# Optimization experiments

Hardware: AMD Instinct MI355X
Metric: run time of the kernel (lower is better)

Reference implementation:

```python
import jax, jax.numpy as jnp
import numpy as np

N_CODES = 4096
D = 256


def setup_inputs() -> dict:
    key = jax.random.key(0)
    k_v, k_w = jax.random.split(key)
    v = jax.random.normal(k_v, (8, 2048, D), dtype=jnp.float32)
    # Embedding init ~ N(0,1), then softmax over dim=1, then row 0 set to 1/d (empty feature)
    w = jax.random.normal(k_w, (N_CODES, D), dtype=jnp.float32)
    w = jax.nn.softmax(w, axis=1)
    w = w.at[0].set(1.0 / D)
    return {"v": v, "vectors": w}


def reference(v, vectors):
    n, d = vectors.shape
    cb = vectors[1:]  # exclude the fixed empty feature at index 0
    # ||v - c||^2 = ||v||^2 - 2 v.c + ||c||^2  (avoids [..., n, d] intermediate)
    v2 = jnp.sum(v * v, axis=-1, keepdims=True)              # [..., 1]
    c2 = jnp.sum(cb * cb, axis=-1)                           # [n-1]
    diff = v2 - 2.0 * jnp.einsum('...d,nd->...n', v, cb) + c2  # [..., n-1]
    idx = jnp.argmin(diff, axis=-1) + 1                      # [...]
    # empty-feature mask: any component differs from 1/d
    mask = jnp.any(v != (1.0 / d), axis=-1)
    idx = jnp.where(mask, idx, 0)
    out = vectors[idx]                                       # gather == onehot @ vectors
    loss = jnp.mean(jnp.square(out - jax.lax.stop_gradient(v)))
    used = jnp.array(0, dtype=jnp.int32)  # eval mode: usage pool is empty
    return out, idx, loss, used
```

## Files before the change

kernel.cpp:

```cpp
#include <hip/hip_runtime.h>
#include <hip/hip_fp16.h>
#include <math.h>
#include <stdint.h>


#define M_TOTAL 16384
#define NCODES  4096
#define D_DIM   256

#define OUT_OFF_IDX  (M_TOTAL * D_DIM)
#define OUT_OFF_LOSS (OUT_OFF_IDX + M_TOTAL)

typedef _Float16 half8 __attribute__((ext_vector_type(8)));
typedef float    float16v __attribute__((ext_vector_type(16)));

__device__ __forceinline__ void gload_lds16(const void* g, void* l) {
  __builtin_amdgcn_global_load_lds(
      (const __attribute__((address_space(1))) void*)g,
      (__attribute__((address_space(3))) void*)l, 16, 0, 0);
}

__global__ __launch_bounds__(256) void prep_kernel(
    const float* __restrict__ V, const float* __restrict__ W,
    _Float16* __restrict__ Vp, _Float16* __restrict__ Bp,
    float* __restrict__ v2, float* __restrict__ c2,
    uint64_t* __restrict__ pk)
{
  __shared__ float T[16 * 264];
  const int t = threadIdx.x;
  const int rloc = t >> 4, seg = t & 15;
  const bool isW = blockIdx.x < 256;
  const int bid2 = isW ? blockIdx.x : (blockIdx.x - 256);
  const int row = bid2 * 16 + rloc;
  const float* X = isW ? W : V;

  if (!isW && bid2 < 64) pk[bid2 * 256 + t] = ~0ULL;

  const float* src = X + (size_t)row * D_DIM + seg * 16;
  float4 x[4];
#pragma unroll
  for (int u = 0; u < 4; ++u) x[u] = ((const float4*)src)[u];
  union { half8 v; _Float16 e[8]; } uh[2], ul[2];
#pragma unroll
  for (int u = 0; u < 4; ++u) {
    float e4[4] = {x[u].x, x[u].y, x[u].z, x[u].w};
#pragma unroll
    for (int j = 0; j < 4; ++j) {
      const int e = u * 4 + j;
      float s = e4[j] * 1024.0f;
      _Float16 h = (_Float16)s;
      uh[e >> 3].e[e & 7] = h;
      ul[e >> 3].e[e & 7] = (_Float16)(s - (float)h);
    }
    *(float4*)&T[rloc * 264 + seg * 16 + u * 4] = x[u];
  }
  if (isW) {
    const int panel = row >> 5, nin = row & 31;
    _Float16* dst = Bp + ((size_t)panel * 16 + seg) * 2048 + nin * 8;
#pragma unroll
    for (int lh = 0; lh < 2; ++lh) {
      *(half8*)(dst + lh * 256)        = uh[lh].v;
      *(half8*)(dst + 1024 + lh * 256) = ul[lh].v;
    }
  } else {
    _Float16* dst = Vp + ((size_t)(row >> 5) * 16 + seg) * 1024 + (row & 31) * 8;
#pragma unroll
    for (int lh = 0; lh < 2; ++lh) {
      *(half8*)(dst + lh * 256)        = uh[lh].v;
      *(half8*)(dst + 512 + lh * 256)  = ul[lh].v;
    }
  }
  __syncthreads();
  const int half = (t >> 3) & 1, j = t & 7;
  const float* tr = &T[rloc * 264 + half * 128 + j];
  float r = __fmul_rn(tr[0], tr[0]);
#pragma unroll
  for (int i = 1; i < 16; ++i) { float e = tr[8 * i]; r = __fadd_rn(r, __fmul_rn(e, e)); }
  r = __fadd_rn(r, __shfl_xor(r, 1));
  r = __fadd_rn(r, __shfl_xor(r, 2));
  r = __fadd_rn(r, __shfl_xor(r, 4));
  r = __fadd_rn(r, __shfl_xor(r, 8));
  if ((t & 15) == 0) { if (isW) c2[row] = r; else v2[row] = r; }
}

__global__ __launch_bounds__(256, 2) void vq_mfma_kernel(
    const _Float16* __restrict__ Vp, const _Float16* __restrict__ Bp,
    const float* __restrict__ v2, const float* __restrict__ c2,
    uint64_t* __restrict__ pk)
{
  __shared__ __align__(16) char smem[77824];
  uint64_t* red2 = (uint64_t*)(smem + 73728);

  const int tid  = threadIdx.x;
  const int lane = tid & 63;
  const int wave = tid >> 6;
  const int wr = wave >> 1, wc = wave & 1;
  const int l31 = lane & 31, lhi = lane >> 5;

  const int bid = blockIdx.x;
  const int xcd  = bid & 7;
  const int seq  = bid >> 3;
  const int mblk = xcd * 8 + (seq & 7);
  const int pblk = seq >> 3;
  const int m0 = mblk * 256;
  const int n0 = pblk * 128;

  const char* gsrc[6];
  int gstr[6], dstOff[6];
#pragma unroll
  for (int j = 0; j < 6; ++j) {
    const int c = wave * 6 + j;
    dstOff[j] = c * 1024;
    if (c < 16) {
      const int p = c >> 1, pl = c & 1;
      gsrc[j] = (const char*)Vp + ((size_t)(mblk * 8 + p) * 16) * 2048 + pl * 1024 + lane * 16;
      gstr[j] = 2048;
    } else {
      const int b = c - 16, pn = b >> 1, pl = b & 1;
      gsrc[j] = (const char*)Bp + ((size_t)(pblk * 4 + pn) * 16) * 4096 + pl * 2048 + lane * 16;
      gstr[j] = 4096;
    }
  }

  auto STAGE2 = [&](int kst, int j0) {
#pragma unroll
    for (int j = j0; j < j0 + 2; ++j) {
      gload_lds16(gsrc[j], smem + (kst % 3) * 24576 + dstOff[j]);
      gsrc[j] += gstr[j];
    }
  };
  auto STAGEFULL = [&](int kst) {
#pragma unroll
    for (int j = 0; j < 6; ++j) {
      gload_lds16(gsrc[j], smem + (kst % 3) * 24576 + dstOff[j]);
      gsrc[j] += gstr[j];
    }
  };

  float16v acc[4][2];
#pragma unroll
  for (int mb = 0; mb < 4; ++mb)
#pragma unroll
    for (int nb = 0; nb < 2; ++nb) acc[mb][nb] = (float16v)0.0f;

  STAGEFULL(0);
  STAGEFULL(1);
  asm volatile("s_waitcnt vmcnt(6)" ::: "memory");
  __builtin_amdgcn_sched_barrier(0);
  __builtin_amdgcn_s_barrier();
  __builtin_amdgcn_sched_barrier(0);

#pragma unroll
  for (int k = 0; k < 16; ++k) {
    const char* Ab = smem + (k % 3) * 24576 + (wr * 4) * 2048 + lane * 16;
    const char* Bb = smem + (k % 3) * 24576 + 16384 + (wc * 2) * 2048 + lane * 16;
    half8 ah[4], al[4], bh[2], bl[2];

#pragma unroll
    for (int mb = 0; mb < 4; ++mb) ah[mb] = *(const half8*)(Ab + mb * 2048);
#pragma unroll
    for (int nb = 0; nb < 2; ++nb) bh[nb] = *(const half8*)(Bb + nb * 2048);
    if (k <= 13) STAGE2(k + 2, 0);
    asm volatile("s_waitcnt lgkmcnt(0)" ::: "memory");
    __builtin_amdgcn_sched_barrier(0);
    __builtin_amdgcn_s_setprio(1);
#pragma unroll
    for (int nb = 0; nb < 2; ++nb)
#pragma unroll
      for (int mb = 0; mb < 4; ++mb)
        acc[mb][nb] = __builtin_amdgcn_mfma_f32_32x32x16_f16(ah[mb], bh[nb], acc[mb][nb], 0, 0, 0);
    __builtin_amdgcn_s_setprio(0);
    __builtin_amdgcn_sched_barrier(0);

#pragma unroll
    for (int nb = 0; nb < 2; ++nb) bl[nb] = *(const half8*)(Bb + nb * 2048 + 1024);
    if (k <= 13) STAGE2(k + 2, 2);
    asm volatile("s_waitcnt lgkmcnt(0)" ::: "memory");
    __builtin_amdgcn_sched_barrier(0);
    __builtin_amdgcn_s_setprio(1);
#pragma unroll
    for (int nb = 0; nb < 2; ++nb)
#pragma unroll
      for (int mb = 0; mb < 4; ++mb)
        acc[mb][nb] = __builtin_amdgcn_mfma_f32_32x32x16_f16(ah[mb], bl[nb], acc[mb][nb], 0, 0, 0);
    __builtin_amdgcn_s_setprio(0);
    __builtin_amdgcn_sched_barrier(0);

#pragma unroll
    for (int mb = 0; mb < 4; ++mb) al[mb] = *(const half8*)(Ab + mb * 2048 + 1024);
    if (k <= 13) STAGE2(k + 2, 4);
    asm volatile("s_waitcnt lgkmcnt(0)" ::: "memory");
    __builtin_amdgcn_sched_barrier(0);
    __builtin_amdgcn_s_setprio(1);
#pragma unroll
    for (int nb = 0; nb < 2; ++nb)
#pragma unroll
      for (int mb = 0; mb < 4; ++mb)
        acc[mb][nb] = __builtin_amdgcn_mfma_f32_32x32x16_f16(al[mb], bh[nb], acc[mb][nb], 0, 0, 0);
    __builtin_amdgcn_s_setprio(0);
    __builtin_amdgcn_sched_barrier(0);

    if (k <= 13)      asm volatile("s_waitcnt vmcnt(6)" ::: "memory");
    else if (k == 14) asm volatile("s_waitcnt vmcnt(0)" ::: "memory");
    if (k < 15) {
      __builtin_amdgcn_sched_barrier(0);
      __builtin_amdgcn_s_barrier();
      __builtin_amdgcn_sched_barrier(0);
    }
  }
  __syncthreads();

  float c2r[2];
#pragma unroll
  for (int nb = 0; nb < 2; ++nb) c2r[nb] = c2[n0 + wc * 64 + nb * 32 + l31];

  uint64_t* wbuf = (uint64_t*)smem + wave * 1056;

#pragma unroll
  for (int mb = 0; mb < 4; ++mb) {
#pragma unroll
    for (int r = 0; r < 16; ++r) {
      const int rowin = (r & 3) + 8 * (r >> 2) + 4 * lhi;
      const float v2m = v2[m0 + wr * 128 + mb * 32 + rowin];
      uint64_t b = ~0ULL;
#pragma unroll
      for (int nb = 0; nb < 2; ++nb) {
        const int n = n0 + wc * 64 + nb * 32 + l31;
        float dot = acc[mb][nb][r] * 0x1p-20f;
        float dd  = __fadd_rn(__fsub_rn(v2m, 2.0f * dot), c2r[nb]);
        if (n == 0) dd = INFINITY;
        uint64_t p = ((uint64_t)__float_as_uint(dd) << 32) | (uint32_t)n;
        if (p < b) b = p;
      }
      wbuf[(r * 2 + lhi) * 33 + l31] = b;
    }
    {
      const int f = lane >> 1, hf = lane & 1;
      const uint64_t* rp = wbuf + f * 33 + hf * 16;
      uint64_t m = rp[0];
#pragma unroll
      for (int i = 1; i < 16; ++i) { uint64_t v = rp[i]; if (v < m) m = v; }
      uint64_t o = __shfl_xor((unsigned long long)m, 1);
      if (o < m) m = o;
      if (hf == 0) {
        const int r_ = f >> 1, lh2 = f & 1;
        const int rowin = (r_ & 3) + 8 * (r_ >> 2) + 4 * lh2;
        red2[(wr * 128 + mb * 32 + rowin) * 2 + wc] = m;
      }
    }
  }
  __syncthreads();

  uint64_t a0 = red2[tid * 2], a1 = red2[tid * 2 + 1];
  atomicMin((unsigned long long*)&pk[m0 + tid], (unsigned long long)(a0 < a1 ? a0 : a1));
}

__global__ __launch_bounds__(256) void gather_kernel(
    const float* __restrict__ V, const float* __restrict__ W,
    const uint64_t* __restrict__ pk,
    float* __restrict__ out, float* __restrict__ outIdx,
    float* __restrict__ lossPartial)
{
  const int q = blockIdx.x * 4 + (threadIdx.x >> 6);
  const int l = threadIdx.x & 63;
  const uint64_t b = pk[q];
  float4 vv = *(const float4*)(V + (size_t)q * D_DIM + l * 4);
  const float inv = 0.00390625f;
  bool ne = (vv.x != inv) | (vv.y != inv) | (vv.z != inv) | (vv.w != inv);
  const int idx = __ballot(ne) ? (int)(uint32_t)b : 0;
  float4 o4 = *(const float4*)(W + (size_t)idx * D_DIM + l * 4);
  *(float4*)(out + (size_t)q * D_DIM + l * 4) = o4;
  if (l == 0) outIdx[q] = (float)idx;
  float dx = o4.x - vv.x, dy = o4.y - vv.y, dz = o4.z - vv.z, dw = o4.w - vv.w;
  float s = dx * dx + dy * dy + dz * dz + dw * dw;
#pragma unroll
  for (int off = 32; off; off >>= 1) s += __shfl_xor(s, off);
  if (l == 0) lossPartial[q] = s;
}

__global__ __launch_bounds__(256) void finalize_kernel(
    const float* __restrict__ lossPartial, float* __restrict__ out)
{
  const int t = threadIdx.x;
  __shared__ float red[256];
  float s = 0.0f;
  for (int i = t; i < M_TOTAL; i += 256) s += lossPartial[i];
  red[t] = s;
  __syncthreads();
  for (int st = 128; st > 0; st >>= 1) {
    if (t < st) red[t] += red[t + st];
    __syncthreads();
  }
  if (t == 0) {
    out[0] = (float)((double)red[0] / (double)(M_TOTAL * D_DIM));
    out[1] = 0.0f;
  }
}

extern "C" void kernel_launch(void* const* d_in, const int* in_sizes, int n_in,
                              void* d_out, int out_size, void* d_ws, size_t ws_size,
                              hipStream_t stream) {
  const float* V = (const float*)d_in[0];
  const float* W = (const float*)d_in[1];
  float* out = (float*)d_out;

  _Float16* Vp = (_Float16*)d_out;

  char* ws = (char*)d_ws;
  _Float16* Bp  = (_Float16*)(ws);
  float*    c2  = (float*)(ws + 8388608);
  float*    v2  = (float*)(ws + 8388608 + 16384);
  uint64_t* pk  = (uint64_t*)(ws + 8388608 + 16384 + 65536);
  float* lossPartial = (float*)(ws + 8388608 + 16384 + 65536 + 131072);

  prep_kernel<<<1280, 256, 0, stream>>>(V, W, Vp, Bp, v2, c2, pk);
  vq_mfma_kernel<<<2048, 256, 0, stream>>>(Vp, Bp, v2, c2, pk);
  gather_kernel<<<M_TOTAL / 4, 256, 0, stream>>>(V, W, pk, out, out + OUT_OFF_IDX, lossPartial);
  finalize_kernel<<<1, 256, 0, stream>>>(lossPartial, out + OUT_OFF_LOSS);
}
```

Before: 192.5 us.

## Enlarge VQ MFMA block tile to 256x256 with 8 waves and per-phase barriers

The distance GEMM block grows from 256x128 to 256x256 codes, using 512 threads (8 waves in a 2x4 grid) and half as many blocks. Each block now reuses its staged V tile across twice as many codebook columns, cutting global and LDS fill traffic per output. The load work is rebalanced so each wave issues four async global-to-LDS copies per k-step. Workgroup barriers are added between the MFMA phases to keep waves in lockstep. In exchange, LDS grows to about 104 KB per block, which likely limits residency to one block per CU, and the extra barriers add synchronisation stalls.

```diff
diff --git a/kernel.cpp b/kernel.cpp
--- a/kernel.cpp
+++ b/kernel.cpp
@@ -83,18 +83,18 @@
   if ((t & 15) == 0) { if (isW) c2[row] = r; else v2[row] = r; }
 }
 
-__global__ __launch_bounds__(256, 2) void vq_mfma_kernel(
+__global__ __launch_bounds__(512, 2) void vq_mfma_kernel(
     const _Float16* __restrict__ Vp, const _Float16* __restrict__ Bp,
     const float* __restrict__ v2, const float* __restrict__ c2,
     uint64_t* __restrict__ pk)
 {
-  __shared__ __align__(16) char smem[77824];
-  uint64_t* red2 = (uint64_t*)(smem + 73728);
+  __shared__ __align__(16) char smem[106496];
+  uint64_t* red2 = (uint64_t*)(smem + 98304);
 
   const int tid  = threadIdx.x;
   const int lane = tid & 63;
   const int wave = tid >> 6;
-  const int wr = wave >> 1, wc = wave & 1;
+  const int wr = wave >> 2, wc = wave & 3;
   const int l31 = lane & 31, lhi = lane >> 5;
 
   const int bid = blockIdx.x;
@@ -103,37 +103,36 @@
   const int mblk = xcd * 8 + (seq & 7);
   const int pblk = seq >> 3;
   const int m0 = mblk * 256;
-  const int n0 = pblk * 128;
-
-  const char* gsrc[6];
-  int gstr[6], dstOff[6];
-#pragma unroll
-  for (int j = 0; j < 6; ++j) {
-    const int c = wave * 6 + j;
-    dstOff[j] = c * 1024;
-    if (c < 16) {
-      const int p = c >> 1, pl = c & 1;
+  const int n0 = pblk * 256;
+
+  const char* gsrc[4];
+  int dstOff[4];
+  const int gstr = (wave < 4) ? 2048 : 4096;
+#pragma unroll
+  for (int j = 0; j < 4; ++j) {
+    if (wave < 4) {
+      const int c = wave * 4 + j, p = c >> 1, pl = c & 1;
       gsrc[j] = (const char*)Vp + ((size_t)(mblk * 8 + p) * 16) * 2048 + pl * 1024 + lane * 16;
-      gstr[j] = 2048;
+      dstOff[j] = c * 1024;
     } else {
-      const int b = c - 16, pn = b >> 1, pl = b & 1;
-      gsrc[j] = (const char*)Bp + ((size_t)(pblk * 4 + pn) * 16) * 4096 + pl * 2048 + lane * 16;
-      gstr[j] = 4096;
+      const int b = (wave - 4) * 4 + j, pn = b >> 1, pl = b & 1;
+      gsrc[j] = (const char*)Bp + ((size_t)(pblk * 8 + pn) * 16) * 4096 + pl * 2048 + lane * 16;
+      dstOff[j] = 16384 + b * 1024;
     }
   }
 
   auto STAGE2 = [&](int kst, int j0) {
 #pragma unroll
     for (int j = j0; j < j0 + 2; ++j) {
-      gload_lds16(gsrc[j], smem + (kst % 3) * 24576 + dstOff[j]);
-      gsrc[j] += gstr[j];
+      gload_lds16(gsrc[j], smem + (kst % 3) * 32768 + dstOff[j]);
+      gsrc[j] += gstr;
     }
   };
   auto STAGEFULL = [&](int kst) {
 #pragma unroll
-    for (int j = 0; j < 6; ++j) {
-      gload_lds16(gsrc[j], smem + (kst % 3) * 24576 + dstOff[j]);
-      gsrc[j] += gstr[j];
+    for (int j = 0; j < 4; ++j) {
+      gload_lds16(gsrc[j], smem + (kst % 3) * 32768 + dstOff[j]);
+      gsrc[j] += gstr;
     }
   };
 
@@ -145,15 +144,15 @@
 
   STAGEFULL(0);
   STAGEFULL(1);
-  asm volatile("s_waitcnt vmcnt(6)" ::: "memory");
+  asm volatile("s_waitcnt vmcnt(4)" ::: "memory");
   __builtin_amdgcn_sched_barrier(0);
   __builtin_amdgcn_s_barrier();
   __builtin_amdgcn_sched_barrier(0);
 
 #pragma unroll
   for (int k = 0; k < 16; ++k) {
-    const char* Ab = smem + (k % 3) * 24576 + (wr * 4) * 2048 + lane * 16;
-    const char* Bb = smem + (k % 3) * 24576 + 16384 + (wc * 2) * 2048 + lane * 16;
+    const char* Ab = smem + (k % 3) * 32768 + (wr * 4) * 2048 + lane * 16;
+    const char* Bb = smem + (k % 3) * 32768 + 16384 + (wc * 2) * 2048 + lane * 16;
     half8 ah[4], al[4], bh[2], bl[2];
 
 #pragma unroll
@@ -161,6 +160,7 @@
 #pragma unroll
     for (int nb = 0; nb < 2; ++nb) bh[nb] = *(const half8*)(Bb + nb * 2048);
     if (k <= 13) STAGE2(k + 2, 0);
+    __builtin_amdgcn_s_barrier();
     asm volatile("s_waitcnt lgkmcnt(0)" ::: "memory");
     __builtin_amdgcn_sched_barrier(0);
     __builtin_amdgcn_s_setprio(1);
@@ -170,11 +170,12 @@
       for (int mb = 0; mb < 4; ++mb)
         acc[mb][nb] = __builtin_amdgcn_mfma_f32_32x32x16_f16(ah[mb], bh[nb], acc[mb][nb], 0, 0, 0);
     __builtin_amdgcn_s_setprio(0);
-    __builtin_amdgcn_sched_barrier(0);
+    __builtin_amdgcn_s_barrier();
 
 #pragma unroll
     for (int nb = 0; nb < 2; ++nb) bl[nb] = *(const half8*)(Bb + nb * 2048 + 1024);
     if (k <= 13) STAGE2(k + 2, 2);
+    __builtin_amdgcn_s_barrier();
     asm volatile("s_waitcnt lgkmcnt(0)" ::: "memory");
     __builtin_amdgcn_sched_barrier(0);
     __builtin_amdgcn_s_setprio(1);
@@ -184,11 +185,11 @@
       for (int mb = 0; mb < 4; ++mb)
         acc[mb][nb] = __builtin_amdgcn_mfma_f32_32x32x16_f16(ah[mb], bl[nb], acc[mb][nb], 0, 0, 0);
     __builtin_amdgcn_s_setprio(0);
-    __builtin_amdgcn_sched_barrier(0);
+    __builtin_amdgcn_s_barrier();
 
 #pragma unroll
     for (int mb = 0; mb < 4; ++mb) al[mb] = *(const half8*)(Ab + mb * 2048 + 1024);
-    if (k <= 13) STAGE2(k + 2, 4);
+    __builtin_amdgcn_s_barrier();
     asm volatile("s_waitcnt lgkmcnt(0)" ::: "memory");
     __builtin_amdgcn_sched_barrier(0);
     __builtin_amdgcn_s_setprio(1);
@@ -198,12 +199,11 @@
       for (int mb = 0; mb < 4; ++mb)
         acc[mb][nb] = __builtin_amdgcn_mfma_f32_32x32x16_f16(al[mb], bh[nb], acc[mb][nb], 0, 0, 0);
     __builtin_amdgcn_s_setprio(0);
+
+    if (k <= 13)      asm volatile("s_waitcnt vmcnt(4)" ::: "memory");
+    else if (k == 14) asm volatile("s_waitcnt vmcnt(0)" ::: "memory");
     __builtin_amdgcn_sched_barrier(0);
-
-    if (k <= 13)      asm volatile("s_waitcnt vmcnt(6)" ::: "memory");
-    else if (k == 14) asm volatile("s_waitcnt vmcnt(0)" ::: "memory");
     if (k < 15) {
-      __builtin_amdgcn_sched_barrier(0);
       __builtin_amdgcn_s_barrier();
       __builtin_amdgcn_sched_barrier(0);
     }
@@ -245,14 +245,18 @@
       if (hf == 0) {
         const int r_ = f >> 1, lh2 = f & 1;
         const int rowin = (r_ & 3) + 8 * (r_ >> 2) + 4 * lh2;
-        red2[(wr * 128 + mb * 32 + rowin) * 2 + wc] = m;
+        red2[(wr * 128 + mb * 32 + rowin) * 4 + wc] = m;
       }
     }
   }
   __syncthreads();
 
-  uint64_t a0 = red2[tid * 2], a1 = red2[tid * 2 + 1];
-  atomicMin((unsigned long long*)&pk[m0 + tid], (unsigned long long)(a0 < a1 ? a0 : a1));
+  if (tid < 256) {
+    uint64_t a = red2[tid * 4];
+#pragma unroll
+    for (int j = 1; j < 4; ++j) { uint64_t v = red2[tid * 4 + j]; if (v < a) a = v; }
+    atomicMin((unsigned long long*)&pk[m0 + tid], (unsigned long long)a);
+  }
 }
 
 __global__ __launch_bounds__(256) void gather_kernel(
@@ -314,7 +318,7 @@
   float* lossPartial = (float*)(ws + 8388608 + 16384 + 65536 + 131072);
 
   prep_kernel<<<1280, 256, 0, stream>>>(V, W, Vp, Bp, v2, c2, pk);
-  vq_mfma_kernel<<<2048, 256, 0, stream>>>(Vp, Bp, v2, c2, pk);
+  vq_mfma_kernel<<<1024, 512, 0, stream>>>(Vp, Bp, v2, c2, pk);
   gather_kernel<<<M_TOTAL / 4, 256, 0, stream>>>(V, W, pk, out, out + OUT_OFF_IDX, lossPartial);
   finalize_kernel<<<1, 256, 0, stream>>>(lossPartial, out + OUT_OFF_LOSS);
 }
```

Result: slower. 205.9 us (+7.0%).
